# Kernel tuning notes

Measured on AMD Instinct MI355X. Metric: run time of the kernel, lower is better.

Reference implementation:

```python
import jax, jax.numpy as jnp
import numpy as np

H = 2048          # hidden_size
I_MOE = 1408      # moe_intermediate_size (per expert)
I_SH = 5632       # shared_expert_intermediate_size
E = 8             # num_experts
TOP_K = 2         # num_experts_per_tok
B, S = 1, 2048


def setup_inputs() -> dict:
    key = jax.random.key(0)
    ks = jax.random.split(key, 7)
    sc = 0.02
    return {
        "hidden_states": jax.random.normal(ks[0], (B, S, H), jnp.float32),
        "W_router": jax.random.normal(ks[1], (E, H), jnp.float32) * sc,      # gate.weight
        "W_sgate": jax.random.normal(ks[2], (1, H), jnp.float32) * sc,       # shared_expert_gate.weight
        "Ws_gate_up": jax.random.normal(ks[3], (H, 2 * I_SH), jnp.float32) * sc,  # shared expert merged gate/up
        "Ws_down": jax.random.normal(ks[4], (I_SH, H), jnp.float32) * sc,
        "We_gate_up": jax.random.normal(ks[5], (E, H, 2 * I_MOE), jnp.float32) * sc,  # stacked expert gate/up
        "We_down": jax.random.normal(ks[6], (E, I_MOE, H), jnp.float32) * sc,
    }


def _silu_and_mul(gu, inter):
    # gate_up layout: [..., 2*inter] -> silu(gate) * up, matching SiluAndMul
    return jax.nn.silu(gu[..., :inter]) * gu[..., inter:]


def reference(hidden_states, W_router, W_sgate, Ws_gate_up, Ws_down, We_gate_up, We_down):
    orig_shape = hidden_states.shape
    x = hidden_states.reshape(-1, H)                     # [T, H]
    T = x.shape[0]

    # --- router: softmax in fp32 then top-k (NOT renormalized, as in source) ---
    logits = x @ W_router.T                              # [T, E]
    probs = jax.nn.softmax(logits.astype(jnp.float32), axis=-1)
    rw, sel = jax.lax.top_k(probs, TOP_K)                # [T, K]
    rw = rw.astype(x.dtype)

    # sparse combine matrix [T, E]: routing weight where selected, else 0
    combine = jnp.zeros((T, E), x.dtype).at[jnp.arange(T)[:, None], sel].add(rw)

    # --- shared expert ---
    sh = _silu_and_mul(x @ Ws_gate_up, I_SH) @ Ws_down    # [T, H]
    shared_out = sh * jax.nn.sigmoid(x @ W_sgate.T)       # [T, H]

    # --- experts: dense dispatch (math-identical to gather/MLP/index_add loop) ---
    gu = jnp.einsum('th,ehi->eti', x, We_gate_up)         # [E, T, 2*I_MOE]
    h = _silu_and_mul(gu, I_MOE)                          # [E, T, I_MOE]
    eo = jnp.einsum('eti,eih->eth', h, We_down)           # [E, T, H]
    sparse_out = jnp.einsum('eth,te->th', eo, combine)    # [T, H]

    return (shared_out + sparse_out).reshape(orig_shape)
```

## Files before the change

kernel.cpp:

```cpp
#include <hip/hip_runtime.h>
#include <cstdio>


#define H_DIM 2048
#define IMOE  1408
#define ISH   5632
#define NEXP  8
#define T_TOK 2048
#define TK_TOT (T_TOK * 2)

typedef __attribute__((ext_vector_type(8))) short short8;
typedef __attribute__((ext_vector_type(8))) __bf16 bf16x8;
typedef __attribute__((ext_vector_type(4))) float f32x4;

__device__ __forceinline__ float bf2f(unsigned short u) {
  union { unsigned int i; float f; } v; v.i = ((unsigned int)u) << 16; return v.f;
}
__device__ __forceinline__ unsigned short f2bf(float f) {
  union { float f; unsigned int i; } v; v.f = f;
  unsigned int x = v.i;
  return (unsigned short)((x + 0x7fffu + ((x >> 16) & 1u)) >> 16);
}

__device__ __forceinline__ f32x4 MFMA16(short8 a, short8 b, f32x4 c) {
  return __builtin_amdgcn_mfma_f32_16x16x32_bf16(
      __builtin_bit_cast(bf16x8, a), __builtin_bit_cast(bf16x8, b), c, 0, 0, 0);
}

__device__ __forceinline__ void gload_lds16(const unsigned short* g, unsigned short* l) {
  __builtin_amdgcn_global_load_lds(
      (const __attribute__((address_space(1))) unsigned int*)g,
      (__attribute__((address_space(3))) unsigned int*)l, 16, 0, 0);
}

__device__ __forceinline__ float silu_f(float x) { return x / (1.0f + __expf(-x)); }

#define SBAR()   asm volatile("s_barrier" ::: "memory")
#define VMCNT(n) asm volatile("s_waitcnt vmcnt(" #n ")" ::: "memory")
#define LGKM0()  asm volatile("s_waitcnt lgkmcnt(0)" ::: "memory")
#define DSR(dst, a) asm volatile("ds_read_b128 %0, %1" : "=v"(dst) : "v"(a))


__global__ __launch_bounds__(256)
void transpose_cvt_kernel(const float* __restrict__ src, unsigned short* __restrict__ dst,
                          int R, int C, long sStride, long dStride) {
  src += (long)blockIdx.z * sStride;
  dst += (long)blockIdx.z * dStride;
  __shared__ float tile[32][33];
  int tx = threadIdx.x, ty = threadIdx.y;
  int x = blockIdx.x * 32 + tx;
  int yb = blockIdx.y * 32;
#pragma unroll
  for (int j = 0; j < 4; j++) {
    int y = yb + ty + j * 8;
    tile[ty + j * 8][tx] = src[(long)y * C + x];
  }
  __syncthreads();
  int c = blockIdx.x * 32 + ty;
  int r = yb + tx;
#pragma unroll
  for (int j = 0; j < 4; j++) {
    dst[(long)(c + j * 8) * R + r] = f2bf(tile[tx][ty + j * 8]);
  }
}

__global__ __launch_bounds__(256)
void cvt_x_kernel(const float* __restrict__ x, unsigned short* __restrict__ xb, int total4) {
  int i = blockIdx.x * 256 + threadIdx.x;
  if (i >= total4) return;
  float4 v = ((const float4*)x)[i];
  ushort4 o;
  o.x = f2bf(v.x); o.y = f2bf(v.y); o.z = f2bf(v.z); o.w = f2bf(v.w);
  ((ushort4*)xb)[i] = o;
}


__global__ __launch_bounds__(256)
void router_kernel(const float* __restrict__ x, const float* __restrict__ Wr,
                   const float* __restrict__ Wsg, float* __restrict__ rw,
                   int* __restrict__ sel, float* __restrict__ sgate_sig,
                   int* __restrict__ counts) {
  int t = blockIdx.x;
  const float* xr = x + (long)t * H_DIM;
  float p[9];
#pragma unroll
  for (int e = 0; e < 9; e++) p[e] = 0.0f;
  for (int h = threadIdx.x; h < H_DIM; h += 256) {
    float xv = xr[h];
#pragma unroll
    for (int e = 0; e < 8; e++) p[e] += xv * Wr[e * H_DIM + h];
    p[8] += xv * Wsg[h];
  }
#pragma unroll
  for (int e = 0; e < 9; e++)
    for (int off = 32; off > 0; off >>= 1)
      p[e] += __shfl_down(p[e], off, 64);
  __shared__ float red[4][9];
  int wave = threadIdx.x >> 6, lane = threadIdx.x & 63;
  if (lane == 0) {
#pragma unroll
    for (int e = 0; e < 9; e++) red[wave][e] = p[e];
  }
  __syncthreads();
  if (threadIdx.x == 0) {
    float lg[9];
#pragma unroll
    for (int e = 0; e < 9; e++) lg[e] = red[0][e] + red[1][e] + red[2][e] + red[3][e];
    float m = lg[0];
#pragma unroll
    for (int e = 1; e < 8; e++) m = fmaxf(m, lg[e]);
    float pr[8], s = 0.0f;
#pragma unroll
    for (int e = 0; e < 8; e++) { pr[e] = expf(lg[e] - m); s += pr[e]; }
    float inv = 1.0f / s;
#pragma unroll
    for (int e = 0; e < 8; e++) pr[e] *= inv;
    int i0 = 0;
#pragma unroll
    for (int e = 1; e < 8; e++) if (pr[e] > pr[i0]) i0 = e;
    int i1 = (i0 == 0) ? 1 : 0;
#pragma unroll
    for (int e = 0; e < 8; e++) if (e != i0 && pr[e] > pr[i1]) i1 = e;
    rw[t * 2] = pr[i0]; rw[t * 2 + 1] = pr[i1];
    sel[t * 2] = i0;    sel[t * 2 + 1] = i1;
    sgate_sig[t] = 1.0f / (1.0f + expf(-lg[8]));
    atomicAdd(&counts[i0], 1);
    atomicAdd(&counts[i1], 1);
  }
}

__global__ void scan_kernel(const int* __restrict__ counts, int* __restrict__ offsets) {
  if (threadIdx.x == 0 && blockIdx.x == 0) {
    int s = 0;
    for (int e = 0; e < NEXP; e++) { offsets[e] = s; s += counts[e]; }
    offsets[NEXP] = s;
  }
}

__global__ __launch_bounds__(256)
void scatter_kernel(const int* __restrict__ sel, const int* __restrict__ offsets,
                    int* __restrict__ cursor, int* __restrict__ tok_of_slot,
                    int* __restrict__ slot_of_tok) {
  int t = blockIdx.x * 256 + threadIdx.x;
  if (t >= T_TOK) return;
#pragma unroll
  for (int k = 0; k < 2; k++) {
    int e = sel[t * 2 + k];
    int pos = atomicAdd(&cursor[e], 1);
    int slot = offsets[e] + pos;
    tok_of_slot[slot] = t;
    slot_of_tok[t * 2 + k] = slot;
  }
}

__global__ __launch_bounds__(256)
void gather_kernel(const unsigned short* __restrict__ xbf, const int* __restrict__ tok,
                   unsigned short* __restrict__ xg) {
  int i = blockIdx.x * 256 + threadIdx.x;
  int slot = i >> 8, c8 = i & 255;
  long src = (long)tok[slot] * H_DIM + c8 * 8;
  ulonglong2 v = *(const ulonglong2*)(xbf + src);
  ((ulonglong2*)xg)[i] = v;
}

template <int PHASE>
__global__ __launch_bounds__(512, 2)
void moe_gemm8_kernel(const unsigned short* __restrict__ Ash,
                      const unsigned short* __restrict__ Bsh,
                      const unsigned short* __restrict__ Aex,
                      const unsigned short* __restrict__ Bex,
                      void* __restrict__ Csh, void* __restrict__ Cex,
                      const int* __restrict__ counts,
                      const int* __restrict__ offsets,
                      const float* __restrict__ rowscale) {
  int o = blockIdx.x;
  int b = (o & 7) * (gridDim.x >> 3) + (o >> 3);

  const unsigned short *A, *B;
  char* Cc;
  int N, Kld, NT, row0, col0, rowbase = 0, cnt, k0 = 0;
  int epi;
  if constexpr (PHASE == 0) {
    if (b < 352) {
      A = Ash; B = Bsh; Cc = (char*)Csh; epi = 0;
      N = 2 * ISH; Kld = H_DIM; NT = H_DIM / 64;
      row0 = (b & 7) * 256; col0 = (b >> 3) * 256; cnt = T_TOK;
    } else {
      int b2 = b - 352, e = b2 / 88, r2 = b2 % 88;
      cnt = counts[e]; row0 = (r2 & 7) * 256;
      if (row0 >= cnt) return;
      rowbase = offsets[e];
      A = Aex; B = Bex + (long)e * 2 * IMOE * H_DIM; Cc = (char*)Cex; epi = 0;
      N = 2 * IMOE; Kld = H_DIM; NT = H_DIM / 64;
      col0 = (r2 >> 3) * 256;
    }
  } else {
    if (b < 256) {
      A = Ash; B = Bsh; Cc = (char*)Csh; epi = 1;
      N = H_DIM; Kld = ISH; NT = (ISH / 4) / 64;
      row0 = (b & 7) * 256; col0 = ((b >> 3) & 7) * 256; cnt = T_TOK;
      k0 = (b >> 6) * (ISH / 4);
    } else {
      int b2 = b - 256, e = b2 >> 6, r2 = b2 & 63;
      cnt = counts[e]; row0 = (r2 & 7) * 256;
      if (row0 >= cnt) return;
      rowbase = offsets[e];
      A = Aex; B = Bex + (long)e * H_DIM * IMOE; Cc = (char*)Cex; epi = 2;
      N = H_DIM; Kld = IMOE; NT = IMOE / 64;
      col0 = (r2 >> 3) * 256;
    }
  }

  __shared__ unsigned short lds8[65536];

  int tid = threadIdx.x, wave = tid >> 6, lane = tid & 63;
  int wr = wave >> 2, wc = wave & 3;
  int fr = lane & 15, fg = lane >> 4;

  unsigned ldsbase = (unsigned)(size_t)lds8;
  unsigned sK0 = (unsigned)(((fg) ^ (fr & 7)) * 16);
  unsigned sK1 = (unsigned)(((4 + fg) ^ (fr & 7)) * 16);
  unsigned aBk0 = ldsbase + (unsigned)(wr * 16384 + fr * 128) + sK0;
  unsigned aBk1 = ldsbase + (unsigned)(wr * 16384 + fr * 128) + sK1;
  unsigned bBk0 = ldsbase + 65536u + (unsigned)((wc >> 1) * 16384 + (wc & 1) * 8192 + fr * 128) + sK0;
  unsigned bBk1 = ldsbase + 65536u + (unsigned)((wc >> 1) * 16384 + (wc & 1) * 8192 + fr * 128) + sK1;

  const unsigned short *pA[2][2], *pB[2][2];
#pragma unroll
  for (int h = 0; h < 2; h++)
#pragma unroll
    for (int s = 0; s < 2; s++) {
      int hr = s * 64 + wave * 8 + (lane >> 3);
      int g = (lane & 7) ^ (hr & 7);
      long ra = row0 + h * 128 + hr;
      if (ra > cnt - 1) ra = cnt - 1;
      ra += rowbase;
      pA[h][s] = A + ra * (long)Kld + k0 + g * 8;
      pB[h][s] = B + (long)(col0 + h * 128 + hr) * Kld + k0 + g * 8;
    }

#define STG_A(d, h, tile) do { long ko = (long)(tile) * 64; \
    gload_lds16(pA[h][0] + ko, &lds8[(d)*16384 + (h)*8192 + wave*512]); \
    gload_lds16(pA[h][1] + ko, &lds8[(d)*16384 + (h)*8192 + 4096 + wave*512]); } while (0)
#define STG_B(d, h, tile) do { long ko = (long)(tile) * 64; \
    gload_lds16(pB[h][0] + ko, &lds8[32768 + (d)*16384 + (h)*8192 + wave*512]); \
    gload_lds16(pB[h][1] + ko, &lds8[32768 + (d)*16384 + (h)*8192 + 4096 + wave*512]); } while (0)

  short8 aReg[4][2], bReg[4][2];
  f32x4 acc[8][4] = {};

#define LDA(mh, d) do { _Pragma("unroll") for (int mi = 0; mi < 4; mi++) { \
      DSR(aReg[mi][0], aBk0 + (unsigned)((d)*32768 + ((mh)*4 + mi)*2048)); \
      DSR(aReg[mi][1], aBk1 + (unsigned)((d)*32768 + ((mh)*4 + mi)*2048)); } } while (0)
#define LDB(nh, d) do { _Pragma("unroll") for (int ni = 0; ni < 2; ni++) { \
      DSR(bReg[(nh)*2 + ni][0], bBk0 + (unsigned)((d)*32768 + ((nh)*2 + ni)*2048)); \
      DSR(bReg[(nh)*2 + ni][1], bBk1 + (unsigned)((d)*32768 + ((nh)*2 + ni)*2048)); } } while (0)
#define MM(mh, nh) do { _Pragma("unroll") for (int mi = 0; mi < 4; mi++) \
    _Pragma("unroll") for (int ni = 0; ni < 2; ni++) \
    _Pragma("unroll") for (int k = 0; k < 2; k++) \
      acc[(mh)*4 + mi][(nh)*2 + ni] = \
          MFMA16(aReg[mi][k], bReg[(nh)*2 + ni][k], acc[(mh)*4 + mi][(nh)*2 + ni]); } while (0)
#define PH_MID() do { SBAR(); LGKM0(); __builtin_amdgcn_sched_barrier(0); \
                      __builtin_amdgcn_s_setprio(1); } while (0)
#define PH_END() do { __builtin_amdgcn_s_setprio(0); SBAR(); } while (0)

  STG_B(0, 0, 0); STG_B(0, 1, 0);
  STG_A(0, 0, 0); STG_A(0, 1, 0);
  STG_B(1, 0, 1); STG_B(1, 1, 1);
  VMCNT(4);
  SBAR();

  int NI = NT >> 1;
  for (int i = 0; i < NI; i++) {
    int t1 = 2 * i + 1;
    int t2 = 2 * i + 2; if (t2 > NT - 1) t2 = NT - 1;
    int t3 = 2 * i + 3; if (t3 > NT - 1) t3 = NT - 1;
    LDA(0, 0); LDB(0, 0); STG_A(1, 0, t1);
    PH_MID(); MM(0, 0); PH_END();
    LDB(1, 0); STG_A(1, 1, t1);
    PH_MID(); MM(0, 1); PH_END();
    LDA(1, 0); STG_B(0, 0, t2);
    PH_MID(); MM(1, 0); PH_END();
    STG_B(0, 1, t2);
    PH_MID(); MM(1, 1);
    __builtin_amdgcn_s_setprio(0); VMCNT(4); SBAR();
    LDA(0, 1); LDB(0, 1); STG_A(0, 0, t2);
    PH_MID(); MM(0, 0); PH_END();
    LDB(1, 1); STG_A(0, 1, t2);
    PH_MID(); MM(0, 1); PH_END();
    LDA(1, 1); STG_B(1, 0, t3);
    PH_MID(); MM(1, 0); PH_END();
    STG_B(1, 1, t3);
    PH_MID(); MM(1, 1);
    __builtin_amdgcn_s_setprio(0); VMCNT(4); SBAR();
  }
  VMCNT(0);

  int rowguard = cnt - row0;
#pragma unroll
  for (int m = 0; m < 8; m++) {
    int rl = wr * 128 + m * 16 + fg * 4;
#pragma unroll
    for (int n = 0; n < 4; n++) {
      int cg = col0 + wc * 64 + n * 16 + fr;
      f32x4 v = acc[m][n];
#pragma unroll
      for (int j = 0; j < 4; j++) {
        int r = rl + j;
        if (r < rowguard) {
          long orow = (long)rowbase + row0 + r;
          long ci = orow * (long)N + cg;
          if (epi == 0)      ((unsigned short*)Cc)[ci] = f2bf(v[j]);
          else if (epi == 1) unsafeAtomicAdd(&((float*)Cc)[ci], v[j] * rowscale[orow]);
          else               ((float*)Cc)[ci] = v[j];
        }
      }
    }
  }
#undef STG_A
#undef STG_B
#undef LDA
#undef LDB
#undef MM
#undef PH_MID
#undef PH_END
}


__global__ __launch_bounds__(256)
void silu2_kernel(const unsigned short* __restrict__ gu_sh, unsigned short* __restrict__ h_sh,
                  const unsigned short* __restrict__ gu_e, unsigned short* __restrict__ h_e) {
  int i = blockIdx.x * 256 + threadIdx.x;
  const int nsh = T_TOK * (ISH / 4);
  const unsigned short* g;
  unsigned short* h;
  int I, row, c4;
  if (i < nsh) {
    g = gu_sh; h = h_sh; I = ISH;
    row = i / (ISH / 4); c4 = i - row * (ISH / 4);
  } else {
    int j = i - nsh;
    g = gu_e; h = h_e; I = IMOE;
    row = j / (IMOE / 4); c4 = j - row * (IMOE / 4);
  }
  const unsigned short* gp = g + (long)row * 2 * I + c4 * 4;
  ushort4 gv = *(const ushort4*)gp;
  ushort4 uv = *(const ushort4*)(gp + I);
  ushort4 o2;
  o2.x = f2bf(silu_f(bf2f(gv.x)) * bf2f(uv.x));
  o2.y = f2bf(silu_f(bf2f(gv.y)) * bf2f(uv.y));
  o2.z = f2bf(silu_f(bf2f(gv.z)) * bf2f(uv.z));
  o2.w = f2bf(silu_f(bf2f(gv.w)) * bf2f(uv.w));
  *(ushort4*)(h + (long)row * I + c4 * 4) = o2;
}

__global__ __launch_bounds__(256)
void combine_kernel(float* __restrict__ out, const float* __restrict__ eo,
                    const int* __restrict__ slot_of_tok, const float* __restrict__ rw) {
  int i = blockIdx.x * 256 + threadIdx.x;
  const int h4n = H_DIM / 4;
  if (i >= T_TOK * h4n) return;
  int t = i / h4n;
  int h4 = i - t * h4n;
  int s0 = slot_of_tok[t * 2], s1 = slot_of_tok[t * 2 + 1];
  float w0 = rw[t * 2], w1 = rw[t * 2 + 1];
  float4 o = ((float4*)out)[i];
  float4 a = ((const float4*)eo)[(long)s0 * h4n + h4];
  float4 b = ((const float4*)eo)[(long)s1 * h4n + h4];
  o.x += w0 * a.x + w1 * b.x;
  o.y += w0 * a.y + w1 * b.y;
  o.z += w0 * a.z + w1 * b.z;
  o.w += w0 * a.w + w1 * b.w;
  ((float4*)out)[i] = o;
}


extern "C" void kernel_launch(void* const* d_in, const int* in_sizes, int n_in,
                              void* d_out, int out_size, void* d_ws, size_t ws_size,
                              hipStream_t stream) {
  (void)in_sizes; (void)n_in; (void)out_size;
  const float* x    = (const float*)d_in[0];
  const float* Wr   = (const float*)d_in[1];
  const float* Wsg  = (const float*)d_in[2];
  const float* Wsgu = (const float*)d_in[3];
  const float* Wsd  = (const float*)d_in[4];
  const float* Wegu = (const float*)d_in[5];
  const float* Wed  = (const float*)d_in[6];
  float* out = (float*)d_out;

  char* ws = (char*)d_ws;
  size_t off = 0;
  auto alloc = [&](size_t b) { size_t o = off; off += (b + 255) & ~(size_t)255; return o; };

  size_t o_xbf   = alloc((size_t)T_TOK * H_DIM * 2);
  size_t o_WsguT = alloc((size_t)2 * ISH * H_DIM * 2);
  size_t o_WsdT  = alloc((size_t)H_DIM * ISH * 2);
  size_t o_WeguT = alloc((size_t)NEXP * 2 * IMOE * H_DIM * 2);
  size_t o_WedT  = alloc((size_t)NEXP * H_DIM * IMOE * 2);
  size_t o_gush  = alloc((size_t)T_TOK * 2 * ISH * 2);
  size_t o_hsh   = alloc((size_t)T_TOK * ISH * 2);
  size_t o_gue   = alloc((size_t)TK_TOT * 2 * IMOE * 2);
  size_t o_xg    = alloc((size_t)TK_TOT * H_DIM * 2);
  size_t o_ints  = alloc(256);
  size_t o_rw    = alloc((size_t)TK_TOT * 4);
  size_t o_sel   = alloc((size_t)TK_TOT * 4);
  size_t o_sg    = alloc((size_t)T_TOK * 4);
  size_t o_tok   = alloc((size_t)TK_TOT * 4);
  size_t o_s2t   = alloc((size_t)TK_TOT * 4);

  if (off > ws_size) {
    fprintf(stderr, "[moe kernel] workspace too small: need %zu have %zu\n", off, ws_size);
    return;
  }

  unsigned short* xbf   = (unsigned short*)(ws + o_xbf);
  unsigned short* WsguT = (unsigned short*)(ws + o_WsguT);
  unsigned short* WsdT  = (unsigned short*)(ws + o_WsdT);
  unsigned short* WeguT = (unsigned short*)(ws + o_WeguT);
  unsigned short* WedT  = (unsigned short*)(ws + o_WedT);
  unsigned short* gu_sh = (unsigned short*)(ws + o_gush);
  unsigned short* h_sh  = (unsigned short*)(ws + o_hsh);
  unsigned short* gu_e  = (unsigned short*)(ws + o_gue);
  unsigned short* xg    = (unsigned short*)(ws + o_xg);
  unsigned short* h_e   = (unsigned short*)(ws + o_WeguT);
  float* eo             = (float*)(ws + o_WsguT);

  int* counts  = (int*)(ws + o_ints);
  int* cursor  = counts + 8;
  int* offsets = counts + 16;
  float* rw    = (float*)(ws + o_rw);
  int* sel     = (int*)(ws + o_sel);
  float* sgate = (float*)(ws + o_sg);
  int* tok     = (int*)(ws + o_tok);
  int* s2t     = (int*)(ws + o_s2t);

  dim3 tb(32, 8, 1);

  hipMemsetAsync(counts, 0, 64, stream);
  hipMemsetAsync(out, 0, (size_t)T_TOK * H_DIM * 4, stream);

  transpose_cvt_kernel<<<dim3(2 * ISH / 32, H_DIM / 32, 1), tb, 0, stream>>>(
      Wsgu, WsguT, H_DIM, 2 * ISH, 0, 0);
  transpose_cvt_kernel<<<dim3(H_DIM / 32, ISH / 32, 1), tb, 0, stream>>>(
      Wsd, WsdT, ISH, H_DIM, 0, 0);
  transpose_cvt_kernel<<<dim3(2 * IMOE / 32, H_DIM / 32, NEXP), tb, 0, stream>>>(
      Wegu, WeguT, H_DIM, 2 * IMOE, (long)H_DIM * 2 * IMOE, (long)2 * IMOE * H_DIM);
  transpose_cvt_kernel<<<dim3(H_DIM / 32, IMOE / 32, NEXP), tb, 0, stream>>>(
      Wed, WedT, IMOE, H_DIM, (long)IMOE * H_DIM, (long)H_DIM * IMOE);

  cvt_x_kernel<<<(T_TOK * H_DIM / 4) / 256, 256, 0, stream>>>(x, xbf, T_TOK * H_DIM / 4);

  router_kernel<<<T_TOK, 256, 0, stream>>>(x, Wr, Wsg, rw, sel, sgate, counts);
  scan_kernel<<<1, 64, 0, stream>>>(counts, offsets);
  scatter_kernel<<<(T_TOK + 255) / 256, 256, 0, stream>>>(sel, offsets, cursor, tok, s2t);
  gather_kernel<<<TK_TOT, 256, 0, stream>>>(xbf, tok, xg);

  moe_gemm8_kernel<0><<<1056, 512, 0, stream>>>(
      xbf, WsguT, xg, WeguT, gu_sh, gu_e, counts, offsets, nullptr);

  {
    int total = T_TOK * (ISH / 4) + TK_TOT * (IMOE / 4);
    silu2_kernel<<<total / 256, 256, 0, stream>>>(gu_sh, h_sh, gu_e, h_e);
  }

  moe_gemm8_kernel<1><<<768, 512, 0, stream>>>(
      h_sh, WsdT, h_e, WedT, out, eo, counts, offsets, sgate);

  combine_kernel<<<(T_TOK * H_DIM / 4) / 256, 256, 0, stream>>>(out, eo, s2t, rw);
}
```

Before: 881.1 us.

## Use persistent GEMM kernels with atomic job queue and split-K partial buffers

Replaces the fixed-grid grouped GEMMs with persistent 256-block kernels that pull compact tile jobs from a queue built on device from the expert counts. Empty expert tiles are never launched, and load balance across CUs improves. The shared-expert down projection now uses a 2-way K split written to separate fp32 buffers instead of 4-way atomic adds, and the sigmoid gate scaling moves into the combine kernel, removing the output memset. The LDS staging order in the pipeline is also reshuffled. The costs are a single-thread job-builder kernel, per-job barrier overhead, and an extra partial-buffer read in combine.

```diff
diff --git a/kernel.cpp b/kernel.cpp
--- a/kernel.cpp
+++ b/kernel.cpp
@@ -163,55 +163,43 @@
   ((ulonglong2*)xg)[i] = v;
 }
 
+__global__ void build_jobs_kernel(const int* __restrict__ counts, int* __restrict__ meta,
+                                  int* __restrict__ jobs0, int* __restrict__ jobs1) {
+  if (threadIdx.x != 0 || blockIdx.x != 0) return;
+  int n0 = 0, n1 = 0;
+  for (int c = 0; c < 44; c++)
+    for (int r = 0; r < 8; r++) jobs0[n0++] = (0 << 28) | (r << 8) | c;
+  for (int e = 0; e < NEXP; e++) {
+    int rows = (counts[e] + 255) >> 8;
+    for (int c = 0; c < 11; c++)
+      for (int r = 0; r < rows; r++)
+        jobs0[n0++] = (1 << 28) | (e << 24) | (r << 8) | c;
+  }
+  for (int ks = 0; ks < 2; ks++)
+    for (int c = 0; c < 8; c++)
+      for (int r = 0; r < 8; r++)
+        jobs1[n1++] = (2 << 28) | (ks << 20) | (r << 8) | c;
+  for (int e = 0; e < NEXP; e++) {
+    int rows = (counts[e] + 255) >> 8;
+    for (int c = 0; c < 8; c++)
+      for (int r = 0; r < rows; r++)
+        jobs1[n1++] = (3 << 28) | (e << 24) | (r << 8) | c;
+  }
+  meta[34] = n0; meta[35] = n1;
+}
+
 template <int PHASE>
 __global__ __launch_bounds__(512, 2)
-void moe_gemm8_kernel(const unsigned short* __restrict__ Ash,
-                      const unsigned short* __restrict__ Bsh,
-                      const unsigned short* __restrict__ Aex,
-                      const unsigned short* __restrict__ Bex,
-                      void* __restrict__ Csh, void* __restrict__ Cex,
-                      const int* __restrict__ counts,
-                      const int* __restrict__ offsets,
-                      const float* __restrict__ rowscale) {
-  int o = blockIdx.x;
-  int b = (o & 7) * (gridDim.x >> 3) + (o >> 3);
-
-  const unsigned short *A, *B;
-  char* Cc;
-  int N, Kld, NT, row0, col0, rowbase = 0, cnt, k0 = 0;
-  int epi;
-  if constexpr (PHASE == 0) {
-    if (b < 352) {
-      A = Ash; B = Bsh; Cc = (char*)Csh; epi = 0;
-      N = 2 * ISH; Kld = H_DIM; NT = H_DIM / 64;
-      row0 = (b & 7) * 256; col0 = (b >> 3) * 256; cnt = T_TOK;
-    } else {
-      int b2 = b - 352, e = b2 / 88, r2 = b2 % 88;
-      cnt = counts[e]; row0 = (r2 & 7) * 256;
-      if (row0 >= cnt) return;
-      rowbase = offsets[e];
-      A = Aex; B = Bex + (long)e * 2 * IMOE * H_DIM; Cc = (char*)Cex; epi = 0;
-      N = 2 * IMOE; Kld = H_DIM; NT = H_DIM / 64;
-      col0 = (r2 >> 3) * 256;
-    }
-  } else {
-    if (b < 256) {
-      A = Ash; B = Bsh; Cc = (char*)Csh; epi = 1;
-      N = H_DIM; Kld = ISH; NT = (ISH / 4) / 64;
-      row0 = (b & 7) * 256; col0 = ((b >> 3) & 7) * 256; cnt = T_TOK;
-      k0 = (b >> 6) * (ISH / 4);
-    } else {
-      int b2 = b - 256, e = b2 >> 6, r2 = b2 & 63;
-      cnt = counts[e]; row0 = (r2 & 7) * 256;
-      if (row0 >= cnt) return;
-      rowbase = offsets[e];
-      A = Aex; B = Bex + (long)e * H_DIM * IMOE; Cc = (char*)Cex; epi = 2;
-      N = H_DIM; Kld = IMOE; NT = IMOE / 64;
-      col0 = (r2 >> 3) * 256;
-    }
-  }
-
+void moe_gemm_p(const unsigned short* __restrict__ Ash,
+                const unsigned short* __restrict__ Bsh,
+                const unsigned short* __restrict__ Aex,
+                const unsigned short* __restrict__ Bex,
+                void* __restrict__ Csh, void* __restrict__ Cex,
+                const int* __restrict__ counts, const int* __restrict__ offsets,
+                const int* __restrict__ jobs, int* __restrict__ qhead,
+                const int* __restrict__ meta) {
   __shared__ unsigned short lds8[65536];
+  __shared__ int jsh;
 
   int tid = threadIdx.x, wave = tid >> 6, lane = tid & 63;
   int wr = wave >> 2, wc = wave & 3;
@@ -225,29 +213,60 @@
   unsigned bBk0 = ldsbase + 65536u + (unsigned)((wc >> 1) * 16384 + (wc & 1) * 8192 + fr * 128) + sK0;
   unsigned bBk1 = ldsbase + 65536u + (unsigned)((wc >> 1) * 16384 + (wc & 1) * 8192 + fr * 128) + sK1;
 
-  const unsigned short *pA[2][2], *pB[2][2];
-#pragma unroll
-  for (int h = 0; h < 2; h++)
-#pragma unroll
-    for (int s = 0; s < 2; s++) {
-      int hr = s * 64 + wave * 8 + (lane >> 3);
-      int g = (lane & 7) ^ (hr & 7);
-      long ra = row0 + h * 128 + hr;
-      if (ra > cnt - 1) ra = cnt - 1;
-      ra += rowbase;
-      pA[h][s] = A + ra * (long)Kld + k0 + g * 8;
-      pB[h][s] = B + (long)(col0 + h * 128 + hr) * Kld + k0 + g * 8;
+  int qcnt = meta[PHASE ? 35 : 34];
+
+  for (;;) {
+    __syncthreads();
+    if (tid == 0) jsh = atomicAdd(qhead, 1);
+    __syncthreads();
+    if (jsh >= qcnt) break;
+    int job = jobs[jsh];
+
+    int kind = (job >> 28) & 3, e = (job >> 24) & 15, ks = (job >> 20) & 3;
+    int row0 = ((job >> 8) & 255) << 8;
+    int col0 = (job & 255) << 8;
+    const unsigned short *A, *B;
+    char* Cc;
+    int N, Kld, NT, k0 = 0, cnt = T_TOK, rowbase = 0;
+    if constexpr (PHASE == 0) {
+      if (kind == 0) { A = Ash; B = Bsh; Cc = (char*)Csh; N = 2 * ISH; Kld = H_DIM; NT = 32; }
+      else {
+        cnt = counts[e]; rowbase = offsets[e];
+        A = Aex; B = Bex + (long)e * (2 * IMOE) * H_DIM; Cc = (char*)Cex;
+        N = 2 * IMOE; Kld = H_DIM; NT = 32;
+      }
+    } else {
+      if (kind == 2) {
+        A = Ash; B = Bsh; Cc = (char*)Csh + (size_t)ks * ((size_t)T_TOK * H_DIM * 4);
+        N = H_DIM; Kld = ISH; NT = 44; k0 = ks * (ISH / 2);
+      } else {
+        cnt = counts[e]; rowbase = offsets[e];
+        A = Aex; B = Bex + (long)e * H_DIM * IMOE; Cc = (char*)Cex;
+        N = H_DIM; Kld = IMOE; NT = 22;
+      }
     }
 
-#define STG_A(d, h, tile) do { long ko = (long)(tile) * 64; \
-    gload_lds16(pA[h][0] + ko, &lds8[(d)*16384 + (h)*8192 + wave*512]); \
-    gload_lds16(pA[h][1] + ko, &lds8[(d)*16384 + (h)*8192 + 4096 + wave*512]); } while (0)
-#define STG_B(d, h, tile) do { long ko = (long)(tile) * 64; \
-    gload_lds16(pB[h][0] + ko, &lds8[32768 + (d)*16384 + (h)*8192 + wave*512]); \
-    gload_lds16(pB[h][1] + ko, &lds8[32768 + (d)*16384 + (h)*8192 + 4096 + wave*512]); } while (0)
-
-  short8 aReg[4][2], bReg[4][2];
-  f32x4 acc[8][4] = {};
+    const unsigned short *pA[2][2], *pB[2][2];
+#pragma unroll
+    for (int h = 0; h < 2; h++)
+#pragma unroll
+      for (int s = 0; s < 2; s++) {
+        int hr = s * 64 + wave * 8 + (lane >> 3);
+        int g = (lane & 7) ^ (hr & 7);
+        long ra = row0 + h * 128 + hr;
+        if (ra > cnt - 1) ra = cnt - 1;
+        ra += rowbase;
+        pA[h][s] = A + ra * (long)Kld + k0 + g * 8;
+        pB[h][s] = B + (long)(col0 + h * 128 + hr) * Kld + k0 + g * 8;
+      }
+
+#define SGA(d, h, s, t) gload_lds16(pA[h][s] + (long)(t) * 64, \
+      &lds8[(d) * 16384 + (h) * 8192 + (s) * 4096 + wave * 512])
+#define SGB(d, h, s, t) gload_lds16(pB[h][s] + (long)(t) * 64, \
+      &lds8[32768 + (d) * 16384 + (h) * 8192 + (s) * 4096 + wave * 512])
+
+    short8 aReg[4][2], bReg[4][2];
+    f32x4 acc[8][4] = {};
 
 #define LDA(mh, d) do { _Pragma("unroll") for (int mi = 0; mi < 4; mi++) { \
       DSR(aReg[mi][0], aBk0 + (unsigned)((d)*32768 + ((mh)*4 + mi)*2048)); \
@@ -264,66 +283,68 @@
                       __builtin_amdgcn_s_setprio(1); } while (0)
 #define PH_END() do { __builtin_amdgcn_s_setprio(0); SBAR(); } while (0)
 
-  STG_B(0, 0, 0); STG_B(0, 1, 0);
-  STG_A(0, 0, 0); STG_A(0, 1, 0);
-  STG_B(1, 0, 1); STG_B(1, 1, 1);
-  VMCNT(4);
-  SBAR();
-
-  int NI = NT >> 1;
-  for (int i = 0; i < NI; i++) {
-    int t1 = 2 * i + 1;
-    int t2 = 2 * i + 2; if (t2 > NT - 1) t2 = NT - 1;
-    int t3 = 2 * i + 3; if (t3 > NT - 1) t3 = NT - 1;
-    LDA(0, 0); LDB(0, 0); STG_A(1, 0, t1);
-    PH_MID(); MM(0, 0); PH_END();
-    LDB(1, 0); STG_A(1, 1, t1);
-    PH_MID(); MM(0, 1); PH_END();
-    LDA(1, 0); STG_B(0, 0, t2);
-    PH_MID(); MM(1, 0); PH_END();
-    STG_B(0, 1, t2);
-    PH_MID(); MM(1, 1);
-    __builtin_amdgcn_s_setprio(0); VMCNT(4); SBAR();
-    LDA(0, 1); LDB(0, 1); STG_A(0, 0, t2);
-    PH_MID(); MM(0, 0); PH_END();
-    LDB(1, 1); STG_A(0, 1, t2);
-    PH_MID(); MM(0, 1); PH_END();
-    LDA(1, 1); STG_B(1, 0, t3);
-    PH_MID(); MM(1, 0); PH_END();
-    STG_B(1, 1, t3);
-    PH_MID(); MM(1, 1);
-    __builtin_amdgcn_s_setprio(0); VMCNT(4); SBAR();
-  }
-  VMCNT(0);
-
-  int rowguard = cnt - row0;
-#pragma unroll
-  for (int m = 0; m < 8; m++) {
-    int rl = wr * 128 + m * 16 + fg * 4;
-#pragma unroll
-    for (int n = 0; n < 4; n++) {
-      int cg = col0 + wc * 64 + n * 16 + fr;
-      f32x4 v = acc[m][n];
-#pragma unroll
-      for (int j = 0; j < 4; j++) {
-        int r = rl + j;
-        if (r < rowguard) {
-          long orow = (long)rowbase + row0 + r;
-          long ci = orow * (long)N + cg;
-          if (epi == 0)      ((unsigned short*)Cc)[ci] = f2bf(v[j]);
-          else if (epi == 1) unsafeAtomicAdd(&((float*)Cc)[ci], v[j] * rowscale[orow]);
-          else               ((float*)Cc)[ci] = v[j];
+    SGA(0, 0, 0, 0); SGA(0, 1, 0, 0); SGA(0, 0, 1, 0); SGA(0, 1, 1, 0);
+    SGB(0, 0, 0, 0); SGB(0, 1, 0, 0); SGB(0, 0, 1, 0); SGB(0, 1, 1, 0);
+    SGA(1, 0, 0, 1); SGA(1, 1, 0, 1);
+    SGB(1, 0, 0, 1); SGB(1, 1, 0, 1);
+    SGA(1, 0, 1, 1); SGA(1, 1, 1, 1);
+    VMCNT(6);
+    SBAR();
+
+    int NI = NT >> 1;
+    for (int i = 0; i < NI; i++) {
+      int td1 = 2 * i + 1;
+      int t2 = 2 * i + 2; if (t2 > NT - 1) t2 = NT - 1;
+      int t3 = 2 * i + 3; if (t3 > NT - 1) t3 = NT - 1;
+      LDA(0, 0); LDB(0, 0); SGB(1, 0, 1, td1); SGB(1, 1, 1, td1);
+      PH_MID(); MM(0, 0); PH_END();
+      LDB(1, 0); SGA(0, 0, 0, t2); SGA(0, 1, 0, t2);
+      PH_MID(); MM(0, 1); PH_END();
+      LDA(1, 0); SGB(0, 0, 0, t2); SGB(0, 1, 0, t2);
+      PH_MID(); MM(1, 0); PH_END();
+      SGB(0, 0, 1, t2); SGB(0, 1, 1, t2);
+      PH_MID(); MM(1, 1);
+      __builtin_amdgcn_s_setprio(0); VMCNT(6); SBAR();
+      LDA(0, 1); LDB(0, 1); SGA(0, 0, 1, t2); SGA(0, 1, 1, t2);
+      PH_MID(); MM(0, 0); PH_END();
+      LDB(1, 1); SGA(1, 0, 0, t3); SGA(1, 1, 0, t3);
+      PH_MID(); MM(0, 1); PH_END();
+      LDA(1, 1); SGB(1, 0, 0, t3); SGB(1, 1, 0, t3);
+      PH_MID(); MM(1, 0); PH_END();
+      SGA(1, 0, 1, t3); SGA(1, 1, 1, t3);
+      PH_MID(); MM(1, 1);
+      __builtin_amdgcn_s_setprio(0); VMCNT(6); SBAR();
+    }
+    VMCNT(0);
+
+    int rowguard = cnt - row0;
+#pragma unroll
+    for (int m = 0; m < 8; m++) {
+      int rl = wr * 128 + m * 16 + fg * 4;
+#pragma unroll
+      for (int n = 0; n < 4; n++) {
+        int cg = col0 + wc * 64 + n * 16 + fr;
+        f32x4 v = acc[m][n];
+#pragma unroll
+        for (int j = 0; j < 4; j++) {
+          int r = rl + j;
+          if (r < rowguard) {
+            long orow = (long)rowbase + row0 + r;
+            long ci = orow * (long)N + cg;
+            if constexpr (PHASE == 0) ((unsigned short*)Cc)[ci] = f2bf(v[j]);
+            else                      ((float*)Cc)[ci] = v[j];
+          }
         }
       }
     }
-  }
-#undef STG_A
-#undef STG_B
+#undef SGA
+#undef SGB
 #undef LDA
 #undef LDB
 #undef MM
 #undef PH_MID
 #undef PH_END
+  }
 }
 
 
@@ -355,8 +376,9 @@
 }
 
 __global__ __launch_bounds__(256)
-void combine_kernel(float* __restrict__ out, const float* __restrict__ eo,
-                    const int* __restrict__ slot_of_tok, const float* __restrict__ rw) {
+void combine_kernel(float* __restrict__ out, const float* __restrict__ sp,
+                    const float* __restrict__ eo, const int* __restrict__ slot_of_tok,
+                    const float* __restrict__ rw, const float* __restrict__ sgate) {
   int i = blockIdx.x * 256 + threadIdx.x;
   const int h4n = H_DIM / 4;
   if (i >= T_TOK * h4n) return;
@@ -364,13 +386,16 @@
   int h4 = i - t * h4n;
   int s0 = slot_of_tok[t * 2], s1 = slot_of_tok[t * 2 + 1];
   float w0 = rw[t * 2], w1 = rw[t * 2 + 1];
-  float4 o = ((float4*)out)[i];
+  float sg = sgate[t];
+  float4 p0 = ((const float4*)sp)[i];
+  float4 p1 = ((const float4*)sp)[(T_TOK * H_DIM / 4) + i];
   float4 a = ((const float4*)eo)[(long)s0 * h4n + h4];
   float4 b = ((const float4*)eo)[(long)s1 * h4n + h4];
-  o.x += w0 * a.x + w1 * b.x;
-  o.y += w0 * a.y + w1 * b.y;
-  o.z += w0 * a.z + w1 * b.z;
-  o.w += w0 * a.w + w1 * b.w;
+  float4 o;
+  o.x = sg * (p0.x + p1.x) + w0 * a.x + w1 * b.x;
+  o.y = sg * (p0.y + p1.y) + w0 * a.y + w1 * b.y;
+  o.z = sg * (p0.z + p1.z) + w0 * a.z + w1 * b.z;
+  o.w = sg * (p0.w + p1.w) + w0 * a.w + w1 * b.w;
   ((float4*)out)[i] = o;
 }
 
@@ -407,6 +432,8 @@
   size_t o_sg    = alloc((size_t)T_TOK * 4);
   size_t o_tok   = alloc((size_t)TK_TOT * 4);
   size_t o_s2t   = alloc((size_t)TK_TOT * 4);
+  size_t o_jb0   = alloc(4096 * 4);
+  size_t o_jb1   = alloc(4096 * 4);
 
   if (off > ws_size) {
     fprintf(stderr, "[moe kernel] workspace too small: need %zu have %zu\n", off, ws_size);
@@ -424,20 +451,25 @@
   unsigned short* xg    = (unsigned short*)(ws + o_xg);
   unsigned short* h_e   = (unsigned short*)(ws + o_WeguT);
   float* eo             = (float*)(ws + o_WsguT);
-
-  int* counts  = (int*)(ws + o_ints);
-  int* cursor  = counts + 8;
-  int* offsets = counts + 16;
+  float* sp             = (float*)(ws + o_gush);
+
+  int* ints    = (int*)(ws + o_ints);
+  int* counts  = ints;
+  int* cursor  = ints + 8;
+  int* offsets = ints + 16;
+  int* qh0     = ints + 32;
+  int* qh1     = ints + 33;
   float* rw    = (float*)(ws + o_rw);
   int* sel     = (int*)(ws + o_sel);
   float* sgate = (float*)(ws + o_sg);
   int* tok     = (int*)(ws + o_tok);
   int* s2t     = (int*)(ws + o_s2t);
+  int* jobs0   = (int*)(ws + o_jb0);
+  int* jobs1   = (int*)(ws + o_jb1);
 
   dim3 tb(32, 8, 1);
 
-  hipMemsetAsync(counts, 0, 64, stream);
-  hipMemsetAsync(out, 0, (size_t)T_TOK * H_DIM * 4, stream);
+  hipMemsetAsync(ints, 0, 256, stream);
 
   transpose_cvt_kernel<<<dim3(2 * ISH / 32, H_DIM / 32, 1), tb, 0, stream>>>(
       Wsgu, WsguT, H_DIM, 2 * ISH, 0, 0);
@@ -452,19 +484,20 @@
 
   router_kernel<<<T_TOK, 256, 0, stream>>>(x, Wr, Wsg, rw, sel, sgate, counts);
   scan_kernel<<<1, 64, 0, stream>>>(counts, offsets);
+  build_jobs_kernel<<<1, 64, 0, stream>>>(counts, ints, jobs0, jobs1);
   scatter_kernel<<<(T_TOK + 255) / 256, 256, 0, stream>>>(sel, offsets, cursor, tok, s2t);
   gather_kernel<<<TK_TOT, 256, 0, stream>>>(xbf, tok, xg);
 
-  moe_gemm8_kernel<0><<<1056, 512, 0, stream>>>(
-      xbf, WsguT, xg, WeguT, gu_sh, gu_e, counts, offsets, nullptr);
+  moe_gemm_p<0><<<256, 512, 0, stream>>>(
+      xbf, WsguT, xg, WeguT, gu_sh, gu_e, counts, offsets, jobs0, qh0, ints);
 
   {
     int total = T_TOK * (ISH / 4) + TK_TOT * (IMOE / 4);
     silu2_kernel<<<total / 256, 256, 0, stream>>>(gu_sh, h_sh, gu_e, h_e);
   }
 
-  moe_gemm8_kernel<1><<<768, 512, 0, stream>>>(
-      h_sh, WsdT, h_e, WedT, out, eo, counts, offsets, sgate);
-
-  combine_kernel<<<(T_TOK * H_DIM / 4) / 256, 256, 0, stream>>>(out, eo, s2t, rw);
-}
+  moe_gemm_p<1><<<256, 512, 0, stream>>>(
+      h_sh, WsdT, h_e, WedT, sp, eo, counts, offsets, jobs1, qh1, ints);
+
+  combine_kernel<<<(T_TOK * H_DIM / 4) / 256, 256, 0, stream>>>(out, sp, eo, s2t, rw, sgate);
+}
```

Result: faster. 861.8 us (-2.2%).
